# Performance work log

Measured on AMD Instinct MI355X. Metric: run time of the kernel, lower is better.

The kernel has to match this reference:

```python
import jax, jax.numpy as jnp
import numpy as np

K_MASK = -2.3819763e+38
ROPE_BASE = 10000
QUERY_SCALE = 0.08838834764831845  # head_dim ** -0.5, head_dim=128
SOFT_CAP = 50.0
SLIDING_WINDOW = 1024
NUM_HEADS = 32
NUM_KV_HEADS = 8


def apply_rope(inputs, positions, base_frequency=ROPE_BASE):
    # inputs: [B, L, N, H], positions: [B, L]
    head_dim = inputs.shape[-1]
    fraction = 2 * jnp.arange(0, head_dim // 2) / head_dim
    timescale = base_frequency ** fraction
    sinusoid = positions[..., None] / timescale[None, None, :]
    sinusoid = sinusoid[..., None, :]  # [B, L, 1, H/2]
    sin = jnp.sin(sinusoid)
    cos = jnp.cos(sinusoid)
    first, second = jnp.split(inputs, 2, axis=-1)
    out = jnp.concatenate([first * cos - second * sin,
                           second * cos + first * sin], axis=-1)
    return out.astype(inputs.dtype)


def setup_inputs() -> dict:
    key = jax.random.key(0)
    ks = jax.random.split(key, 4)
    B, S, D, N, K, H = 1, 2048, 4096, NUM_HEADS, NUM_KV_HEADS, 128
    x = jax.random.normal(ks[0], (B, S, D), dtype=jnp.float32)
    segment_pos = jnp.broadcast_to(jnp.arange(S, dtype=jnp.int32)[None, :], (B, S))
    # causal mask [B, T, S]
    attn_mask = jnp.broadcast_to(jnp.tril(jnp.ones((S, S), dtype=bool))[None], (B, S, S))
    sd = 1.0 / np.sqrt(D)
    q_w = jax.random.normal(ks[1], (N, D, H), dtype=jnp.float32) * sd
    kv_w = jax.random.normal(ks[2], (2, K, D, H), dtype=jnp.float32) * sd
    out_w = jax.random.normal(ks[3], (N, H, D), dtype=jnp.float32) * (1.0 / np.sqrt(N * H))
    return {"x": x, "segment_pos": segment_pos, "attn_mask": attn_mask,
            "q_w": q_w, "kv_w": kv_w, "out_w": out_w}


def reference(x, segment_pos, attn_mask, q_w, kv_w, out_w):
    B, T, D = x.shape
    N, _, H = q_w.shape
    K = kv_w.shape[1]
    G = N // K

    q = jnp.einsum('BTD,NDH->BTNH', x, q_w)
    k = jnp.einsum('BSD,KDH->BSKH', x, kv_w[0])
    v = jnp.einsum('BSD,KDH->BSKH', x, kv_w[1])

    q = apply_rope(q, segment_pos)
    q = q * QUERY_SCALE
    k = apply_rope(k, segment_pos)

    # GQA logits: [B, T, K, G, S] -> [B, T, N, S]
    qg = q.reshape(B, T, K, G, H)
    logits = jnp.einsum('BTKGH,BSKH->BTKGS', qg, k).reshape(B, T, N, T)

    # soft cap
    logits = jnp.tanh(logits / SOFT_CAP) * SOFT_CAP

    # sliding-window mask (no cache: end_index=0, cache positions = arange)
    cache_positions = jnp.arange(T)[None, None, :]          # [1, 1, S]
    sp = segment_pos[:, :, None]                             # [B, T, 1]
    sliding = (cache_positions > sp - SLIDING_WINDOW) & (cache_positions < sp + SLIDING_WINDOW)
    mask = attn_mask & sliding                               # [B, T, S]

    padded = jnp.where(mask[:, :, None, :], logits, K_MASK)
    probs = jax.nn.softmax(padded, axis=-1).astype(k.dtype)

    pg = probs.reshape(B, T, K, G, T)
    encoded = jnp.einsum('BTKGS,BSKH->BTKGH', pg, v).reshape(B, T, N, H)
    out = jnp.einsum('BTNH,NHD->BTD', encoded, out_w)
    return out
```

## Files before the change

kernel.cpp:

```cpp
#include <hip/hip_runtime.h>
#include <stdint.h>

#define SEQ     2048
#define DMODEL  4096
#define NHEADS  32
#define NKV     8
#define HD      128
#define NQKV    6144
#define K_MASK_F (-2.3819763e+38f)
#define QSCALE   0.08838834764831845f

typedef __attribute__((ext_vector_type(8))) short short8;
typedef __attribute__((ext_vector_type(4))) short short4v;
typedef __attribute__((ext_vector_type(4))) float f32x4;

__device__ __forceinline__ short f2bf(float f) {
  unsigned u = __float_as_uint(f);
  unsigned r = (u + 0x7fffu + ((u >> 16) & 1u)) >> 16;
  return (short)r;
}
__device__ __forceinline__ float bf2f(short s) {
  return __uint_as_float(((unsigned)(unsigned short)s) << 16);
}
__device__ __forceinline__ void split_bf(float v, short& h, short& l) {
  h = f2bf(v);
  l = f2bf(v - bf2f(h));
}
__device__ __forceinline__ f32x4 mfma16(short8 a, short8 b, f32x4 c) {
  return __builtin_amdgcn_mfma_f32_16x16x32_bf16(a, b, c, 0, 0, 0);
}
__device__ __forceinline__ void async16(void* lds, const void* g) {
  __builtin_amdgcn_global_load_lds(
      (const __attribute__((address_space(1))) unsigned int*)g,
      (__attribute__((address_space(3))) unsigned int*)lds, 16, 0, 0);
}
__device__ __forceinline__ float softcap(float s) {
  float e = __expf(s * 0.04f);
  return 50.f - 100.f * __builtin_amdgcn_rcpf(e + 1.f);
}

__global__ void cvt_split_kernel(const float* __restrict__ src, short* __restrict__ hi,
                                 short* __restrict__ lo, int n4) {
  int i = blockIdx.x * blockDim.x + threadIdx.x;
  if (i >= n4) return;
  float4 v = ((const float4*)src)[i];
  float vv[4] = {v.x, v.y, v.z, v.w};
  short hh[4], ll[4];
#pragma unroll
  for (int j = 0; j < 4; ++j) split_bf(vv[j], hh[j], ll[j]);
  short4v h = {hh[0], hh[1], hh[2], hh[3]};
  short4v l = {ll[0], ll[1], ll[2], ll[3]};
  ((short4v*)hi)[i] = h;
  ((short4v*)lo)[i] = l;
}

__global__ void tcvt_kernel(const float* __restrict__ src, long srcSlab, int srcStride,
                            short* __restrict__ dhi, short* __restrict__ dlo,
                            long dstSlab, int dstStride) {
  __shared__ float tile[32][33];
  const float* s = src + (long)blockIdx.z * srcSlab;
  long dbase = (long)blockIdx.z * dstSlab;
  int tx = threadIdx.x & 31, ty = threadIdx.x >> 5;
  int c0 = blockIdx.x * 32, r0 = blockIdx.y * 32;
#pragma unroll
  for (int i = 0; i < 32; i += 8)
    tile[ty + i][tx] = s[(long)(r0 + ty + i) * srcStride + (c0 + tx)];
  __syncthreads();
#pragma unroll
  for (int i = 0; i < 32; i += 8) {
    float v = tile[tx][ty + i];
    long o = dbase + (long)(c0 + ty + i) * dstStride + (r0 + tx);
    short h, l;
    split_bf(v, h, l);
    dhi[o] = h;
    dlo[o] = l;
  }
}

__global__ __launch_bounds__(256)
void gemm3_kernel(const short* __restrict__ Ah, const short* __restrict__ Al,
                  const short* __restrict__ Bh, const short* __restrict__ Bl,
                  float* __restrict__ C, int K, int ldc) {
  __shared__ short lds[4 * 128 * 32];
  const int tid = threadIdx.x;
  const int wave = tid >> 6, lane = tid & 63;
  const int r16 = lane & 15, g4 = lane >> 4;
  const int bm = blockIdx.x, bn = blockIdx.y;
  const int wr = wave >> 1, wc = wave & 1;

  const f32x4 zero = {0.f, 0.f, 0.f, 0.f};
  f32x4 acc[4][4];
#pragma unroll
  for (int m = 0; m < 4; ++m)
#pragma unroll
    for (int n = 0; n < 4; ++n) acc[m][n] = zero;

  const short* gsrc[4] = {Ah, Al, Bh, Bl};
  const int rowbase[4] = {bm * 128, bm * 128, bn * 128, bn * 128};
  const int stgrow = tid >> 2;
  const int stgseg = tid & 3;
  const int nk = K >> 5;

  for (int kt = 0; kt < nk; ++kt) {
    __syncthreads();
#pragma unroll
    for (int b = 0; b < 4; ++b) {
#pragma unroll
      for (int rnd = 0; rnd < 2; ++rnd) {
        int row = rnd * 64 + stgrow;
        const short* g = gsrc[b] + (long)(rowbase[b] + row) * K + kt * 32 + stgseg * 8;
        short* l = lds + b * 4096 + rnd * 2048 + wave * 512;
        async16(l, g);
      }
    }
    __syncthreads();

    short8 afh[4], afl[4], bfh[4], bfl[4];
#pragma unroll
    for (int m = 0; m < 4; ++m) {
      int r = wr * 64 + m * 16 + r16;
      afh[m] = *(const short8*)&lds[0 * 4096 + r * 32 + g4 * 8];
      afl[m] = *(const short8*)&lds[1 * 4096 + r * 32 + g4 * 8];
    }
#pragma unroll
    for (int n = 0; n < 4; ++n) {
      int r = wc * 64 + n * 16 + r16;
      bfh[n] = *(const short8*)&lds[2 * 4096 + r * 32 + g4 * 8];
      bfl[n] = *(const short8*)&lds[3 * 4096 + r * 32 + g4 * 8];
    }
#pragma unroll
    for (int m = 0; m < 4; ++m)
#pragma unroll
      for (int n = 0; n < 4; ++n) {
        acc[m][n] = mfma16(afh[m], bfh[n], acc[m][n]);
        acc[m][n] = mfma16(afh[m], bfl[n], acc[m][n]);
        acc[m][n] = mfma16(afl[m], bfh[n], acc[m][n]);
      }
  }
#pragma unroll
  for (int m = 0; m < 4; ++m)
#pragma unroll
    for (int n = 0; n < 4; ++n) {
      int row = bm * 128 + wr * 64 + m * 16 + g4 * 4;
      int col = bn * 128 + wc * 64 + n * 16 + r16;
#pragma unroll
      for (int r = 0; r < 4; ++r) C[(long)(row + r) * ldc + col] = acc[m][n][r];
    }
}

__global__ void rope_cvt_kernel(const float* __restrict__ qkv, short* __restrict__ qh,
                                short* __restrict__ ql, short* __restrict__ kh,
                                short* __restrict__ kl) {
  int idx = blockIdx.x * 256 + threadIdx.x;
  const int QP = NHEADS * SEQ * 64;
  float first, second, scale;
  long obase;
  int t, hp;
  short *oh, *ol;
  if (idx < QP) {
    int n = idx >> 17;
    int rem = idx & 131071;
    t = rem >> 6;
    hp = rem & 63;
    const float* p = qkv + (long)t * NQKV + n * HD + hp;
    first = p[0];
    second = p[64];
    oh = qh; ol = ql;
    obase = ((long)n * SEQ + t) * HD + hp;
    scale = QSCALE;
  } else {
    int j = idx - QP;
    int kvh = j >> 17;
    int rem = j & 131071;
    t = rem >> 6;
    hp = rem & 63;
    const float* p = qkv + (long)t * NQKV + DMODEL + kvh * HD + hp;
    first = p[0];
    second = p[64];
    oh = kh; ol = kl;
    obase = ((long)kvh * SEQ + t) * HD + hp;
    scale = 1.0f;
  }
  float ts = powf(10000.0f, (float)hp * (1.0f / 64.0f));
  float ang = (float)t / ts;
  float sn, cs;
  sincosf(ang, &sn, &cs);
  float o1 = (first * cs - second * sn) * scale;
  float o2 = (second * cs + first * sn) * scale;
  short h, l;
  split_bf(o1, h, l); oh[obase] = h;      ol[obase] = l;
  split_bf(o2, h, l); oh[obase + 64] = h; ol[obase + 64] = l;
}

#define VCH 1040
__global__ __launch_bounds__(256)
void attn_kernel(const short* __restrict__ qh, const short* __restrict__ ql,
                 const short* __restrict__ kh, const short* __restrict__ kl,
                 const short* __restrict__ vth, const short* __restrict__ vtl,
                 short* __restrict__ ench, short* __restrict__ encl) {
  __shared__ short kt[2][2][32 * 128];
  __shared__ short vlds[2][2][4 * VCH];
  __shared__ short plds[4][2][512];
  const int bx = blockIdx.x;
  const int n = ((bx & 7) << 2) + (bx >> 3);
  const int by = blockIdx.y;
  const int qt = (by < 16) ? (16 + by) : (31 - by);
  const int tid = threadIdx.x;
  const int wave = tid >> 6, lane = tid & 63;
  const int kv = n >> 2;
  const int T0 = qt * 64;
  const int wq0 = T0 + wave * 16;
  const int r16 = lane & 15, g4 = lane >> 4;

  short8 qfh[4], qfl[4];
  {
    const short* bh = qh + ((long)(n * SEQ + wq0 + r16)) * HD + g4 * 8;
    const short* bl = ql + ((long)(n * SEQ + wq0 + r16)) * HD + g4 * 8;
#pragma unroll
    for (int ks = 0; ks < 4; ++ks) {
      qfh[ks] = *(const short8*)(bh + ks * 32);
      qfl[ks] = *(const short8*)(bl + ks * 32);
    }
  }

  const f32x4 zero = {0.f, 0.f, 0.f, 0.f};
  f32x4 o[8];
#pragma unroll
  for (int i = 0; i < 8; ++i) o[i] = zero;
  float lsum[4] = {0.f, 0.f, 0.f, 0.f};

  short* pwh = &plds[wave][0][0];
  short* pwl = &plds[wave][1][0];

  const int strow = tid >> 4;
  const int stcol = (((tid & 15) ^ (strow & 7)) << 3);
  const short* kgh = kh + (long)kv * SEQ * HD;
  const short* kgl = kl + (long)kv * SEQ * HD;
  const short* vgh = vth + (long)kv * HD * SEQ;
  const short* vgl = vtl + (long)kv * HD * SEQ;

  int slo = T0 - 1023;
  if (slo < 0) slo = 0;
  slo &= ~31;
  const int steps = (T0 + 64 - slo) >> 5;

  auto stage = [&](int sc, int kbuf) {
#pragma unroll
    for (int c = 0; c < 2; ++c) {
      int row = c * 16 + strow;
      async16(&kt[kbuf][0][c * 2048 + tid * 8], kgh + (long)(sc + row) * HD + stcol);
      async16(&kt[kbuf][1][c * 2048 + tid * 8], kgl + (long)(sc + row) * HD + stcol);
    }
#pragma unroll
    for (int r = 0; r < 2; ++r) {
      int h = r * 64 + lane;
      async16(&vlds[kbuf][0][wave * VCH + r * 512 + lane * 8],
              vgh + (long)h * SEQ + sc + wave * 8);
      async16(&vlds[kbuf][1][wave * VCH + r * 512 + lane * 8],
              vgl + (long)h * SEQ + sc + wave * 8);
    }
  };

  int buf = 0;
  stage(slo, 0);
  __syncthreads();

  for (int i = 0; i < steps; ++i) {
    const int sc = slo + (i << 5);
    if (i + 1 < steps) stage(sc + 32, buf ^ 1);
    const bool active = (sc <= wq0 + 15) && (sc + 31 >= wq0 - 1023);
    if (active) {
      const short* kb0 = &kt[buf][0][0];
      const short* kb1 = &kt[buf][1][0];
      f32x4 sA0 = zero, sB0 = zero, sA1 = zero, sB1 = zero;
#pragma unroll
      for (int ks = 0; ks < 4; ++ks) {
        const int ca = (ks * 32 + g4 * 8) ^ ((r16 & 7) << 3);
        short8 k0h = *(const short8*)&kb0[r16 * 128 + ca];
        short8 k0l = *(const short8*)&kb1[r16 * 128 + ca];
        short8 k1h = *(const short8*)&kb0[(16 + r16) * 128 + ca];
        short8 k1l = *(const short8*)&kb1[(16 + r16) * 128 + ca];
        sA0 = mfma16(qfh[ks], k0h, sA0);
        sA1 = mfma16(qfh[ks], k1h, sA1);
        sB0 = mfma16(qfh[ks], k0l, sB0);
        sB1 = mfma16(qfh[ks], k1l, sB1);
        sB0 = mfma16(qfl[ks], k0h, sB0);
        sB1 = mfma16(qfl[ks], k1h, sB1);
      }
      float p0[4], p1[4];
#pragma unroll
      for (int r = 0; r < 4; ++r) {
        const int t = wq0 + g4 * 4 + r;
        const float v0 = softcap(sA0[r] + sB0[r]);
        const float v1 = softcap(sA1[r] + sB1[r]);
        const int c0 = sc + r16, c1 = c0 + 16;
        p0[r] = (c0 <= t && c0 > t - 1024) ? __expf(v0 - 50.f) : 0.f;
        p1[r] = (c1 <= t && c1 > t - 1024) ? __expf(v1 - 50.f) : 0.f;
        lsum[r] += p0[r] + p1[r];
      }
#pragma unroll
      for (int r = 0; r < 4; ++r) {
        const int prow = g4 * 4 + r;
        short sh, sl;
        const int off0 = prow * 32 + (((r16 >> 3) ^ (prow & 3)) * 8) + (r16 & 7);
        split_bf(p0[r], sh, sl);
        pwh[off0] = sh;
        pwl[off0] = sl;
        const int off1 = prow * 32 + ((((16 + r16) >> 3) ^ (prow & 3)) * 8) + (r16 & 7);
        split_bf(p1[r], sh, sl);
        pwh[off1] = sh;
        pwl[off1] = sl;
      }
      short8 pah = *(const short8*)&pwh[r16 * 32 + ((g4 ^ (r16 & 3)) * 8)];
      short8 pal = *(const short8*)&pwl[r16 * 32 + ((g4 ^ (r16 & 3)) * 8)];
      const short* vb0 = &vlds[buf][0][0];
      const short* vb1 = &vlds[buf][1][0];
#pragma unroll
      for (int hf = 0; hf < 8; ++hf) {
        const int vo = g4 * VCH + (hf * 16 + r16) * 8;
        short8 vbh = *(const short8*)&vb0[vo];
        short8 vbl = *(const short8*)&vb1[vo];
        o[hf] = mfma16(pah, vbh, o[hf]);
        o[hf] = mfma16(pah, vbl, o[hf]);
        o[hf] = mfma16(pal, vbh, o[hf]);
      }
    }
    __syncthreads();
    buf ^= 1;
  }

  float inv[4];
#pragma unroll
  for (int r = 0; r < 4; ++r) {
    float s = lsum[r];
    s += __shfl_xor(s, 1);
    s += __shfl_xor(s, 2);
    s += __shfl_xor(s, 4);
    s += __shfl_xor(s, 8);
    inv[r] = 1.0f / s;
  }
#pragma unroll
  for (int hf = 0; hf < 8; ++hf)
#pragma unroll
    for (int r = 0; r < 4; ++r) {
      const float val = o[hf][r] * inv[r];
      const int t = wq0 + g4 * 4 + r;
      const long off = (long)t * DMODEL + n * HD + hf * 16 + r16;
      short sh, sl;
      split_bf(val, sh, sl);
      ench[off] = sh;
      encl[off] = sl;
    }
}

extern "C" void kernel_launch(void* const* d_in, const int* in_sizes, int n_in,
                              void* d_out, int out_size, void* d_ws, size_t ws_size,
                              hipStream_t stream) {
  const float* x     = (const float*)d_in[0];
  const float* q_w   = (const float*)d_in[3];
  const float* kv_w  = (const float*)d_in[4];
  const float* out_w = (const float*)d_in[5];
  float* out = (float*)d_out;

  char* w = (char*)d_ws;
  const size_t MB = 1ull << 20;
  short* xh   = (short*)(w + 0);
  short* xl   = (short*)(w + 16 * MB);
  short* W1Th = (short*)(w + 32 * MB);
  short* W1Tl = (short*)(w + 80 * MB);
  short* W2Th = (short*)(w + 32 * MB);
  short* W2Tl = (short*)(w + 64 * MB);
  float* qkv  = (float*)(w + 128 * MB);
  short* ench = (short*)(w + 128 * MB);
  short* encl = (short*)(w + 144 * MB);
  short* qH   = (short*)(w + 176 * MB);
  short* qL   = (short*)(w + 192 * MB);
  short* kH   = (short*)(w + 208 * MB);
  short* kL   = (short*)(w + 212 * MB);
  short* vtH  = (short*)(w + 216 * MB);
  short* vtL  = (short*)(w + 220 * MB);

  cvt_split_kernel<<<8192, 256, 0, stream>>>(x, xh, xl, 2097152);
  tcvt_kernel<<<dim3(4, 128, 32), 256, 0, stream>>>(q_w, (long)4096 * 128, 128,
                                                    W1Th, W1Tl, (long)128 * 4096, 4096);
  tcvt_kernel<<<dim3(4, 128, 8), 256, 0, stream>>>(kv_w, (long)4096 * 128, 128,
                                                   W1Th + (long)4096 * 4096,
                                                   W1Tl + (long)4096 * 4096,
                                                   (long)128 * 4096, 4096);
  tcvt_kernel<<<dim3(4, 128, 8), 256, 0, stream>>>(kv_w + (long)8 * 4096 * 128,
                                                   (long)4096 * 128, 128,
                                                   W1Th + (long)5120 * 4096,
                                                   W1Tl + (long)5120 * 4096,
                                                   (long)128 * 4096, 4096);
  gemm3_kernel<<<dim3(16, 48), 256, 0, stream>>>(xh, xl, W1Th, W1Tl, qkv, 4096, 6144);
  rope_cvt_kernel<<<20480, 256, 0, stream>>>(qkv, qH, qL, kH, kL);
  tcvt_kernel<<<dim3(4, 64, 8), 256, 0, stream>>>(qkv + 5120, 128, 6144,
                                                  vtH, vtL, (long)128 * 2048, 2048);
  attn_kernel<<<dim3(32, 32), 256, 0, stream>>>(qH, qL, kH, kL, vtH, vtL, ench, encl);
  tcvt_kernel<<<dim3(128, 128, 1), 256, 0, stream>>>(out_w, 0, 4096, W2Th, W2Tl, 0, 4096);
  gemm3_kernel<<<dim3(16, 32), 256, 0, stream>>>(ench, encl, W2Th, W2Tl, out, 4096, 4096);
}
```

Measured before the change: 907.6 us.

## Replace GEMM with double-buffered 512-thread kernel using wider N tiles

Replaces the 128x128 split-bf16 GEMM with a templated 512-thread kernel that uses 128xBN tiles (BN=384 for the QKV projection, 256 for the output projection). A/B fragments are double-buffered in dynamic LDS and prefetched two k-steps ahead with async loads and explicit vmcnt waits. Barriers are split per phase, and s_setprio is raised around the MFMA blocks. The aim is to hide global-load latency, cut per-k-step synchronisation, and make each tile reuse more data. In exchange it uses much more LDS (up to 128KB), which limits occupancy, and its hand-tuned waitcnt counts are fragile.

```diff
diff --git a/kernel.cpp b/kernel.cpp
--- a/kernel.cpp
+++ b/kernel.cpp
@@ -77,74 +77,142 @@
   }
 }
 
-__global__ __launch_bounds__(256)
-void gemm3_kernel(const short* __restrict__ Ah, const short* __restrict__ Al,
-                  const short* __restrict__ Bh, const short* __restrict__ Bl,
-                  float* __restrict__ C, int K, int ldc) {
-  __shared__ short lds[4 * 128 * 32];
+template <int BN>
+__global__ __launch_bounds__(512, 2)
+void gemm256_kernel(const short* __restrict__ Ah, const short* __restrict__ Al,
+                    const short* __restrict__ Bh, const short* __restrict__ Bl,
+                    float* __restrict__ C, int K, int ldc) {
+  constexpr int P = BN / 128;
+  constexpr int BN32 = BN * 32;
+  constexpr int BUFS = 8192 + BN * 64;
+  constexpr int CGW = BN / 64;
+  extern __shared__ short lds[];
   const int tid = threadIdx.x;
   const int wave = tid >> 6, lane = tid & 63;
   const int r16 = lane & 15, g4 = lane >> 4;
-  const int bm = blockIdx.x, bn = blockIdx.y;
-  const int wr = wave >> 1, wc = wave & 1;
-
+  const int wr = wave >> 2, wc = wave & 3;
+  const int bm = blockIdx.x & 15, bn = blockIdx.x >> 4;
+  const int NK = K >> 5;
+  const int aoff = g4 * 128 + r16 * 8;
+
+  const short* Apl[2] = {Ah, Al};
+  const short* Bpl[2] = {Bh, Bl};
+
+  auto stageA = [&](int q, int ktT, int bufbit) {
+    const int idx = (wave << 1) | q;
+    const int p = idx >> 3, fg = idx & 7;
+    const short* g = Apl[p] + (long)(bm * 128 + fg * 16 + r16) * K + ktT * 32 + g4 * 8;
+    async16(&lds[bufbit + p * 4096 + fg * 512], g);
+  };
+  auto stageB = [&](int ph, int q, int ktT, int bufbit) {
+    const int idx = (wave << 1) | q;
+    const int p = idx >> 3, e = idx & 7;
+    const int cg = (e >> 1) * CGW + ph * 2 + (e & 1);
+    const short* g = Bpl[p] + (long)(bn * BN + cg * 16 + r16) * K + ktT * 32 + g4 * 8;
+    async16(&lds[bufbit + 8192 + p * BN32 + cg * 512], g);
+  };
+
+  f32x4 acc[4][2 * P];
   const f32x4 zero = {0.f, 0.f, 0.f, 0.f};
-  f32x4 acc[4][4];
-#pragma unroll
-  for (int m = 0; m < 4; ++m)
-#pragma unroll
-    for (int n = 0; n < 4; ++n) acc[m][n] = zero;
-
-  const short* gsrc[4] = {Ah, Al, Bh, Bl};
-  const int rowbase[4] = {bm * 128, bm * 128, bn * 128, bn * 128};
-  const int stgrow = tid >> 2;
-  const int stgseg = tid & 3;
-  const int nk = K >> 5;
-
-  for (int kt = 0; kt < nk; ++kt) {
-    __syncthreads();
-#pragma unroll
-    for (int b = 0; b < 4; ++b) {
-#pragma unroll
-      for (int rnd = 0; rnd < 2; ++rnd) {
-        int row = rnd * 64 + stgrow;
-        const short* g = gsrc[b] + (long)(rowbase[b] + row) * K + kt * 32 + stgseg * 8;
-        short* l = lds + b * 4096 + rnd * 2048 + wave * 512;
-        async16(l, g);
-      }
-    }
-    __syncthreads();
-
-    short8 afh[4], afl[4], bfh[4], bfl[4];
-#pragma unroll
-    for (int m = 0; m < 4; ++m) {
-      int r = wr * 64 + m * 16 + r16;
-      afh[m] = *(const short8*)&lds[0 * 4096 + r * 32 + g4 * 8];
-      afl[m] = *(const short8*)&lds[1 * 4096 + r * 32 + g4 * 8];
-    }
-#pragma unroll
-    for (int n = 0; n < 4; ++n) {
-      int r = wc * 64 + n * 16 + r16;
-      bfh[n] = *(const short8*)&lds[2 * 4096 + r * 32 + g4 * 8];
-      bfl[n] = *(const short8*)&lds[3 * 4096 + r * 32 + g4 * 8];
-    }
-#pragma unroll
-    for (int m = 0; m < 4; ++m)
-#pragma unroll
-      for (int n = 0; n < 4; ++n) {
-        acc[m][n] = mfma16(afh[m], bfh[n], acc[m][n]);
-        acc[m][n] = mfma16(afh[m], bfl[n], acc[m][n]);
-        acc[m][n] = mfma16(afl[m], bfh[n], acc[m][n]);
-      }
-  }
-#pragma unroll
-  for (int m = 0; m < 4; ++m)
-#pragma unroll
-    for (int n = 0; n < 4; ++n) {
-      int row = bm * 128 + wr * 64 + m * 16 + g4 * 4;
-      int col = bn * 128 + wc * 64 + n * 16 + r16;
-#pragma unroll
-      for (int r = 0; r < 4; ++r) C[(long)(row + r) * ldc + col] = acc[m][n][r];
+#pragma unroll
+  for (int mi = 0; mi < 4; ++mi)
+#pragma unroll
+    for (int nf = 0; nf < 2 * P; ++nf) acc[mi][nf] = zero;
+
+  stageA(0, 0, 0);
+  stageA(1, 0, 0);
+#pragma unroll
+  for (int ph = 0; ph < P; ++ph) {
+    stageB(ph, 0, 0, 0);
+    stageB(ph, 1, 0, 0);
+  }
+  stageA(0, 1, BUFS);
+  stageA(1, 1, BUFS);
+#pragma unroll
+  for (int ph = 0; ph < P - 1; ++ph) {
+    stageB(ph, 0, 1, BUFS);
+    stageB(ph, 1, 1, BUFS);
+  }
+  if constexpr (P == 2) asm volatile("s_waitcnt vmcnt(4)" ::: "memory");
+  else                  asm volatile("s_waitcnt vmcnt(6)" ::: "memory");
+  __builtin_amdgcn_sched_barrier(0);
+  __builtin_amdgcn_s_barrier();
+
+  for (int kt = 0; kt < NK; ++kt) {
+    const int bufS = (kt & 1) ? BUFS : 0;
+    const int nbufS = BUFS - bufS;
+    short8 a[4][2];
+#pragma unroll
+    for (int ph = 0; ph < P; ++ph) {
+      short8 b[2][2];
+      if (ph == 0) {
+#pragma unroll
+        for (int mi = 0; mi < 4; ++mi)
+#pragma unroll
+          for (int p = 0; p < 2; ++p)
+            a[mi][p] = *(const short8*)&lds[bufS + p * 4096 + (wr * 4 + mi) * 512 + aoff];
+      }
+#pragma unroll
+      for (int ni = 0; ni < 2; ++ni)
+#pragma unroll
+        for (int p = 0; p < 2; ++p)
+          b[ni][p] = *(const short8*)&lds[bufS + 8192 + p * BN32 +
+                                          (wc * CGW + ph * 2 + ni) * 512 + aoff];
+      if (ph == 0) {
+        if (kt + 1 < NK) {
+          stageB(P - 1, 0, kt + 1, nbufS);
+          stageB(P - 1, 1, kt + 1, nbufS);
+        }
+      } else if (ph == 1) {
+        if (kt + 2 < NK) {
+          stageA(0, kt + 2, bufS);
+          stageA(1, kt + 2, bufS);
+          stageB(0, 0, kt + 2, bufS);
+          stageB(0, 1, kt + 2, bufS);
+        }
+      } else {
+        if (kt + 2 < NK) {
+          stageB(ph - 1, 0, kt + 2, bufS);
+          stageB(ph - 1, 1, kt + 2, bufS);
+        }
+      }
+      __builtin_amdgcn_s_barrier();
+      asm volatile("s_waitcnt lgkmcnt(0)" ::: "memory");
+      __builtin_amdgcn_sched_barrier(0);
+      __builtin_amdgcn_s_setprio(1);
+#pragma unroll
+      for (int mi = 0; mi < 4; ++mi)
+#pragma unroll
+        for (int ni = 0; ni < 2; ++ni) {
+          f32x4 c = acc[mi][ph * 2 + ni];
+          c = mfma16(a[mi][0], b[ni][0], c);
+          c = mfma16(a[mi][0], b[ni][1], c);
+          c = mfma16(a[mi][1], b[ni][0], c);
+          acc[mi][ph * 2 + ni] = c;
+        }
+      __builtin_amdgcn_s_setprio(0);
+      if (ph == P - 1) {
+        if (kt + 2 < NK) {
+          if constexpr (P == 2) asm volatile("s_waitcnt vmcnt(4)" ::: "memory");
+          else                  asm volatile("s_waitcnt vmcnt(6)" ::: "memory");
+        } else {
+          asm volatile("s_waitcnt vmcnt(0)" ::: "memory");
+        }
+        __builtin_amdgcn_sched_barrier(0);
+      }
+      __builtin_amdgcn_s_barrier();
+    }
+  }
+
+#pragma unroll
+  for (int mi = 0; mi < 4; ++mi)
+#pragma unroll
+    for (int nf = 0; nf < 2 * P; ++nf) {
+      const int row = bm * 128 + wr * 64 + mi * 16 + g4 * 4;
+      const int col = bn * BN + wc * (BN / 4) + nf * 16 + r16;
+#pragma unroll
+      for (int rr = 0; rr < 4; ++rr)
+        C[(long)(row + rr) * ldc + col] = acc[mi][nf][rr];
     }
 }
 
@@ -380,6 +448,11 @@
   short* vtH  = (short*)(w + 216 * MB);
   short* vtL  = (short*)(w + 220 * MB);
 
+  hipFuncSetAttribute(reinterpret_cast<const void*>(gemm256_kernel<384>),
+                      hipFuncAttributeMaxDynamicSharedMemorySize, 131072);
+  hipFuncSetAttribute(reinterpret_cast<const void*>(gemm256_kernel<256>),
+                      hipFuncAttributeMaxDynamicSharedMemorySize, 98304);
+
   cvt_split_kernel<<<8192, 256, 0, stream>>>(x, xh, xl, 2097152);
   tcvt_kernel<<<dim3(4, 128, 32), 256, 0, stream>>>(q_w, (long)4096 * 128, 128,
                                                     W1Th, W1Tl, (long)128 * 4096, 4096);
@@ -392,11 +465,13 @@
                                                    W1Th + (long)5120 * 4096,
                                                    W1Tl + (long)5120 * 4096,
                                                    (long)128 * 4096, 4096);
-  gemm3_kernel<<<dim3(16, 48), 256, 0, stream>>>(xh, xl, W1Th, W1Tl, qkv, 4096, 6144);
+  gemm256_kernel<384><<<dim3(256), dim3(512), 131072, stream>>>(
+      xh, xl, W1Th, W1Tl, qkv, 4096, 6144);
   rope_cvt_kernel<<<20480, 256, 0, stream>>>(qkv, qH, qL, kH, kL);
   tcvt_kernel<<<dim3(4, 64, 8), 256, 0, stream>>>(qkv + 5120, 128, 6144,
                                                   vtH, vtL, (long)128 * 2048, 2048);
   attn_kernel<<<dim3(32, 32), 256, 0, stream>>>(qH, qL, kH, kL, vtH, vtL, ench, encl);
   tcvt_kernel<<<dim3(128, 128, 1), 256, 0, stream>>>(out_w, 0, 4096, W2Th, W2Tl, 0, 4096);
-  gemm3_kernel<<<dim3(16, 32), 256, 0, stream>>>(ench, encl, W2Th, W2Tl, out, 4096, 4096);
-}
+  gemm256_kernel<256><<<dim3(256), dim3(512), 98304, stream>>>(
+      ench, encl, W2Th, W2Tl, out, 4096, 4096);
+}
```

Result: faster. 870.0 us (-4.1%).
